# Kernel optimization log

Hardware: AMD Instinct MI355X
Metric: run time of the kernel (lower is better)

The kernel has to match this reference:

```python
import jax, jax.numpy as jnp
import numpy as np

VOCAB, DIM = 100000, 300
B, L = 4096, 200
HIDDEN, OUT = 1000, 3


def setup_inputs() -> dict:
    key = jax.random.key(0)
    k_emb, k_x, k_len, k_w1, k_b1, k_w2, k_b2 = jax.random.split(key, 7)
    emb_table = jax.random.normal(k_emb, (VOCAB, DIM), dtype=jnp.float32)
    x = jax.random.randint(k_x, (B, L), 0, VOCAB)
    lengths = jax.random.randint(k_len, (B,), 1, L + 1)  # >=1 to avoid div-by-zero
    W1 = jax.random.normal(k_w1, (2 * DIM, HIDDEN), dtype=jnp.float32) * 0.02
    b1 = jax.random.normal(k_b1, (HIDDEN,), dtype=jnp.float32) * 0.02
    W2 = jax.random.normal(k_w2, (HIDDEN, OUT), dtype=jnp.float32) * 0.02
    b2 = jax.random.normal(k_b2, (OUT,), dtype=jnp.float32) * 0.02
    return {"emb_table": emb_table, "W1": W1, "b1": b1, "W2": W2, "b2": b2,
            "x": x, "lengths": lengths}


def reference(emb_table, W1, b1, W2, b2, x, lengths):
    emb = emb_table[x]                                   # [B, L, D] gather
    # Faithful to original: mean uses sum over ALL positions (incl. padding)
    mean_pooled = jnp.sum(emb, axis=1) / lengths[:, None].astype(emb.dtype)  # [B, D]
    # Max only over the first `length` real tokens
    mask = jnp.arange(L)[None, :] < lengths[:, None]     # [B, L]
    neg_inf = jnp.array(-jnp.inf, dtype=emb.dtype)
    max_pooled = jnp.max(jnp.where(mask[:, :, None], emb, neg_inf), axis=1)  # [B, D]
    rep = jnp.concatenate([mean_pooled, max_pooled], axis=1)  # [B, 2D]
    h = jax.nn.relu(rep @ W1 + b1)                       # [B, 1000]
    return h @ W2 + b2                                   # [B, OUT]
```

## Files before the change

kernel.cpp:

```cpp
#include <hip/hip_runtime.h>
#include <math.h>

#define VOCAB  100000
#define DIM    300
#define IDIM   320
#define BB     4096
#define LL     200
#define HIDDEN 1000
#define OUTC   3
#define KT     19
#define NT     64
#define MTILES (BB / 16)

#define QSCALE (6.0f / 127.0f)
#define QINV   (127.0f / 6.0f)

#define W1_BLKS   ((KT * NT * 64 + 255) / 256)
#define INIT_BLKS ((BB * OUTC + 255) / 256)
#define CONV_BLKS ((VOCAB * 20 + 255) / 256)

typedef __attribute__((ext_vector_type(8))) short  short8;
typedef __attribute__((ext_vector_type(4))) float  floatx4;
typedef __attribute__((ext_vector_type(2))) unsigned short ushort2v;

__device__ inline ushort f2bf(float f) {
    union { float f; unsigned u; } v; v.f = f;
    unsigned u = v.u;
    u += 0x7fffu + ((u >> 16) & 1u);
    return (ushort)(u >> 16);
}
__device__ inline float4 f4max(float4 a, float4 b) {
    return make_float4(fmaxf(a.x, b.x), fmaxf(a.y, b.y), fmaxf(a.z, b.z), fmaxf(a.w, b.w));
}
__device__ inline float4 f4add(float4 a, float4 b) {
    return make_float4(a.x + b.x, a.y + b.y, a.z + b.z, a.w + b.w);
}
__device__ inline unsigned pkmax16(unsigned a, unsigned b) {
    union { unsigned u; ushort2v v; } x, y, r;
    x.u = a; y.u = b;
    r.v = __builtin_elementwise_max(x.v, y.v);
    return r.u;
}

__device__ inline int a_slot(int k, int ml) {
    const int kt = k >> 5, kk = k & 31;
    return ((kt << 6) + ml + ((kk >> 3) << 4)) * 8 + (kk & 7);
}

__device__ inline unsigned q4(float a, float b, float c, float d) {
    int q0 = min(max(__float2int_rn(a * QINV) + 128, 0), 255);
    int q1 = min(max(__float2int_rn(b * QINV) + 128, 0), 255);
    int q2 = min(max(__float2int_rn(c * QINV) + 128, 0), 255);
    int q3 = min(max(__float2int_rn(d * QINV) + 128, 0), 255);
    return (unsigned)q0 | ((unsigned)q1 << 8) | ((unsigned)q2 << 16) | ((unsigned)q3 << 24);
}

__global__ __launch_bounds__(256) void prep_all(
    const float* __restrict__ emb, unsigned char* __restrict__ embQ,
    const float* __restrict__ W1,  ushort* __restrict__ w1p,
    const float* __restrict__ b2,  float* __restrict__ out)
{
    const int bid = blockIdx.x;
    const int tid = threadIdx.x;
    if (bid < W1_BLKS) {
        const int g = bid * 256 + tid;
        if (g >= KT * NT * 64) return;
        const int lane = g & 63;
        const int nt   = (g >> 6) & (NT - 1);
        const int kt   = g >> 12;
        const int n    = nt * 16 + (lane & 15);
        const int kb   = kt * 32 + ((lane >> 4) << 3);
        short8 v;
        #pragma unroll
        for (int j = 0; j < 8; ++j) {
            const int k = kb + j;
            const float f = (k < 600 && n < HIDDEN) ? W1[k * HIDDEN + n] : 0.f;
            v[j] = (short)f2bf(f);
        }
        ((short8*)w1p)[g] = v;
    } else if (bid < W1_BLKS + INIT_BLKS) {
        const int g = (bid - W1_BLKS) * 256 + tid;
        if (g < BB * OUTC) out[g] = b2[g % OUTC];
    } else {
        const int g = (bid - W1_BLKS - INIT_BLKS) * 256 + tid;
        if (g >= VOCAB * 20) return;
        const int row = g / 20;
        const int c   = g - row * 20;
        const float4* rp = (const float4*)(emb + (size_t)row * DIM);
        uint4 o;
        unsigned* ow = (unsigned*)&o;
        #pragma unroll
        for (int v = 0; v < 4; ++v) {
            const int fi = 4 * c + v;
            float4 f = (fi < 75) ? rp[fi] : make_float4(0.f, 0.f, 0.f, 0.f);
            ow[v] = q4(f.x, f.y, f.z, f.w);
        }
        *(uint4*)(embQ + (size_t)g * 16) = o;
    }
}

__global__ __launch_bounds__(256, 8) void gather_pool_i8(
    const unsigned char* __restrict__ embQ,
    const int*           __restrict__ x,
    const int*           __restrict__ lengths,
    ushort*              __restrict__ repA)
{
    __shared__ int      xS[LL];
    __shared__ unsigned pS[3][20][8];
    __shared__ unsigned pM[3][20][8];

    const int tid  = threadIdx.x;
    const int lane = tid & 63;
    const int wave = tid >> 6;
    const int row  = blockIdx.x;

    for (int i = tid; i < LL; i += 256) xS[i] = x[row * LL + i];
    const int len = lengths[row];
    __syncthreads();

    const int  t0   = wave * 50;
    const int  vmax = min(max(len - t0, 0), 50);
    const bool ga   = (lane < 20);
    const bool ld   = (lane < 40);
    const int  lg   = ga ? lane : (lane - 20);

    unsigned sLo[4], sHi[4], mLo[4], mHi[4];
    #pragma unroll
    for (int w = 0; w < 4; ++w) { sLo[w] = sHi[w] = 0u; mLo[w] = mHi[w] = 0u; }

    uint4 raw = make_uint4(0, 0, 0, 0);
    const int full = vmax >> 1;
    int p = 0;
    for (; p < full; ++p) {
        const int tA  = t0 + 2 * p;
        const int idx = ga ? xS[tA] : xS[tA + 1];
        if (ld) raw = *(const uint4*)(embQ + (size_t)idx * IDIM + 16 * lg);
        const unsigned* ww = (const unsigned*)&raw;
        #pragma unroll
        for (int w = 0; w < 4; ++w) {
            const unsigned u  = ww[w];
            const unsigned lo = u & 0x00FF00FFu;
            const unsigned hi = (u >> 8) & 0x00FF00FFu;
            sLo[w] += lo;  sHi[w] += hi;
            mLo[w] = pkmax16(mLo[w], lo);
            mHi[w] = pkmax16(mHi[w], hi);
        }
    }
    if (vmax & 1) {
        const int tA  = t0 + 2 * p;
        const int idx = ga ? xS[tA] : xS[tA + 1];
        if (ld) raw = *(const uint4*)(embQ + (size_t)idx * IDIM + 16 * lg);
        const unsigned* ww = (const unsigned*)&raw;
        #pragma unroll
        for (int w = 0; w < 4; ++w) {
            const unsigned u  = ww[w];
            const unsigned lo = u & 0x00FF00FFu;
            const unsigned hi = (u >> 8) & 0x00FF00FFu;
            sLo[w] += lo;  sHi[w] += hi;
            if (ga) {
                mLo[w] = pkmax16(mLo[w], lo);
                mHi[w] = pkmax16(mHi[w], hi);
            }
        }
        ++p;
    }
    for (; p < 25; ++p) {
        const int tA  = t0 + 2 * p;
        const int idx = ga ? xS[tA] : xS[tA + 1];
        if (ld) raw = *(const uint4*)(embQ + (size_t)idx * IDIM + 16 * lg);
        const unsigned* ww = (const unsigned*)&raw;
        #pragma unroll
        for (int w = 0; w < 4; ++w) {
            const unsigned u = ww[w];
            sLo[w] += u & 0x00FF00FFu;
            sHi[w] += (u >> 8) & 0x00FF00FFu;
        }
    }

    {
        const int src = ga ? (lane + 20) : lane;
        #pragma unroll
        for (int w = 0; w < 4; ++w) {
            sLo[w] += (unsigned)__shfl((int)sLo[w], src);
            sHi[w] += (unsigned)__shfl((int)sHi[w], src);
            mLo[w] = pkmax16(mLo[w], (unsigned)__shfl((int)mLo[w], src));
            mHi[w] = pkmax16(mHi[w], (unsigned)__shfl((int)mHi[w], src));
        }
    }

    if (wave != 0 && ga) {
        #pragma unroll
        for (int w = 0; w < 4; ++w) {
            pS[wave - 1][lane][w]     = sLo[w];
            pS[wave - 1][lane][4 + w] = sHi[w];
            pM[wave - 1][lane][w]     = mLo[w];
            pM[wave - 1][lane][4 + w] = mHi[w];
        }
    }
    __syncthreads();
    if (wave == 0 && ga) {
        #pragma unroll
        for (int wv = 0; wv < 3; ++wv)
            #pragma unroll
            for (int w = 0; w < 4; ++w) {
                sLo[w] += pS[wv][lane][w];
                sHi[w] += pS[wv][lane][4 + w];
                mLo[w] = pkmax16(mLo[w], pM[wv][lane][w]);
                mHi[w] = pkmax16(mHi[w], pM[wv][lane][4 + w]);
            }

        float s[16], m[16];
        #pragma unroll
        for (int w = 0; w < 4; ++w) {
            s[4*w+0] = (float)(sLo[w] & 0xFFFFu);
            s[4*w+2] = (float)(sLo[w] >> 16);
            s[4*w+1] = (float)(sHi[w] & 0xFFFFu);
            s[4*w+3] = (float)(sHi[w] >> 16);
            m[4*w+0] = (float)(mLo[w] & 0xFFFFu);
            m[4*w+2] = (float)(mLo[w] >> 16);
            m[4*w+1] = (float)(mHi[w] & 0xFFFFu);
            m[4*w+3] = (float)(mHi[w] >> 16);
        }

        const float c1 = QSCALE / (float)len;
        const int mt = row >> 4;
        const int ml = row & 15;
        ushort* rb = repA + (size_t)mt * (KT * 512);

        ushort mv[16];
        #pragma unroll
        for (int j = 0; j < 16; ++j) mv[j] = f2bf((m[j] - 128.f) * QSCALE);

        if (lane < 18) {
            #pragma unroll
            for (int h = 0; h < 2; ++h) {
                short8 q;
                #pragma unroll
                for (int j = 0; j < 8; ++j)
                    q[j] = (short)f2bf((s[8*h + j] - 25600.f) * c1);
                *(short8*)(rb + a_slot(16 * lane + 8 * h, ml)) = q;
            }
            #pragma unroll
            for (int h = 0; h < 2; ++h) {
                const int k0 = 300 + 16 * lane + 8 * h;
                *(ushort4*)(rb + a_slot(k0, ml)) =
                    make_ushort4(mv[8*h+0], mv[8*h+1], mv[8*h+2], mv[8*h+3]);
                *(ushort4*)(rb + a_slot(k0 + 4, ml)) =
                    make_ushort4(mv[8*h+4], mv[8*h+5], mv[8*h+6], mv[8*h+7]);
            }
        } else if (lane == 18) {
            short8 q;
            #pragma unroll
            for (int j = 0; j < 8; ++j) q[j] = (short)f2bf((s[j] - 25600.f) * c1);
            *(short8*)(rb + a_slot(288, ml)) = q;
            *(ushort4*)(rb + a_slot(296, ml)) =
                make_ushort4(f2bf((s[8] - 25600.f) * c1), f2bf((s[9] - 25600.f) * c1),
                             f2bf((s[10] - 25600.f) * c1), f2bf((s[11] - 25600.f) * c1));
            *(ushort4*)(rb + a_slot(588, ml)) = make_ushort4(mv[0], mv[1], mv[2], mv[3]);
            *(ushort4*)(rb + a_slot(592, ml)) = make_ushort4(mv[4], mv[5], mv[6], mv[7]);
            *(ushort4*)(rb + a_slot(596, ml)) = make_ushort4(mv[8], mv[9], mv[10], mv[11]);
            *(ushort4*)(rb + a_slot(600, ml)) = make_ushort4(0, 0, 0, 0);
        } else {
            *(ushort4*)(rb + a_slot(604, ml)) = make_ushort4(0, 0, 0, 0);
        }
    }
}

__global__ __launch_bounds__(256, 8) void gather_pool_f32(
    const float* __restrict__ emb,
    const int*   __restrict__ x,
    const int*   __restrict__ lengths,
    ushort*      __restrict__ repA)
{
    __shared__ int    xS[LL];
    __shared__ float4 pS[3][75];
    __shared__ float4 pM[3][75];

    const int tid  = threadIdx.x;
    const int lane = tid & 63;
    const int wave = tid >> 6;
    const int row  = blockIdx.x;

    for (int i = tid; i < LL; i += 256) xS[i] = x[row * LL + i];
    const int len = lengths[row];
    __syncthreads();

    const int  t0   = wave * (LL / 4);
    const int  vmax = min(max(len - t0, 0), LL / 4);
    const bool tl   = (lane < 11);
    const float4 z4 = make_float4(0.f, 0.f, 0.f, 0.f);

    float4 s4 = z4, st = z4;
    float4 m4 = make_float4(-INFINITY, -INFINITY, -INFINITY, -INFINITY);
    float4 mt = m4;

    int t = 0;
    #pragma unroll 4
    for (; t < vmax; ++t) {
        const int idx = xS[t0 + t];
        const float4* rp = (const float4*)(emb + (size_t)idx * DIM);
        float4 a = rp[lane];
        float4 b = tl ? rp[64 + lane] : z4;
        s4 = f4add(s4, a); st = f4add(st, b);
        m4 = f4max(m4, a); mt = f4max(mt, b);
    }
    #pragma unroll 4
    for (; t < LL / 4; ++t) {
        const int idx = xS[t0 + t];
        const float4* rp = (const float4*)(emb + (size_t)idx * DIM);
        float4 a = rp[lane];
        float4 b = tl ? rp[64 + lane] : z4;
        s4 = f4add(s4, a); st = f4add(st, b);
    }

    if (wave != 0) {
        pS[wave - 1][lane] = s4; pM[wave - 1][lane] = m4;
        if (tl) { pS[wave - 1][64 + lane] = st; pM[wave - 1][64 + lane] = mt; }
    }
    __syncthreads();
    if (wave == 0) {
        #pragma unroll
        for (int w = 0; w < 3; ++w) {
            s4 = f4add(s4, pS[w][lane]); m4 = f4max(m4, pM[w][lane]);
            if (tl) { st = f4add(st, pS[w][64 + lane]); mt = f4max(mt, pM[w][64 + lane]); }
        }
        const float inv = 1.0f / (float)len;
        const int mtile = row >> 4;
        const int ml    = row & 15;
        ushort* rb = repA + (size_t)mtile * (KT * 512);
        {
            ushort4 q = make_ushort4(f2bf(s4.x*inv), f2bf(s4.y*inv), f2bf(s4.z*inv), f2bf(s4.w*inv));
            *(ushort4*)(rb + a_slot(4 * lane, ml)) = q;
        }
        {
            ushort4 q = make_ushort4(f2bf(m4.x), f2bf(m4.y), f2bf(m4.z), f2bf(m4.w));
            *(ushort4*)(rb + a_slot(300 + 4 * lane, ml)) = q;
        }
        if (tl) {
            ushort4 q1 = make_ushort4(f2bf(st.x*inv), f2bf(st.y*inv), f2bf(st.z*inv), f2bf(st.w*inv));
            *(ushort4*)(rb + a_slot(256 + 4 * lane, ml)) = q1;
            ushort4 q2 = make_ushort4(f2bf(mt.x), f2bf(mt.y), f2bf(mt.z), f2bf(mt.w));
            *(ushort4*)(rb + a_slot(556 + 4 * lane, ml)) = q2;
        }
        if (lane >= 56) rb[a_slot(600 + (lane - 56), ml)] = 0;
    }
}

__global__ __launch_bounds__(256, 4) void mlp_mfma(
    const ushort* __restrict__ w1p,
    const ushort* __restrict__ repA,
    const float*  __restrict__ b1,
    const float*  __restrict__ W2,
    float*        __restrict__ out)
{
    __shared__ short8 aS[KT * 64];
    __shared__ float  red[4][16][3];

    const int tid  = threadIdx.x;
    const int lane = tid & 63;
    const int wave = tid >> 6;
    const int mt   = blockIdx.x >> 2;
    const int q    = blockIdx.x & 3;

    {
        const short8* ap = (const short8*)(repA + (size_t)mt * (KT * 512));
        for (int i = tid; i < KT * 64; i += 256) aS[i] = ap[i];
    }
    __syncthreads();

    const int nt0 = q * 16 + wave * 4;
    const short8* bp = (const short8*)w1p;

    floatx4 acc[4];
    #pragma unroll
    for (int s = 0; s < 4; ++s) acc[s] = (floatx4){0.f, 0.f, 0.f, 0.f};

    #pragma unroll
    for (int kt = 0; kt < KT; ++kt) {
        const short8 av = aS[kt * 64 + lane];
        const short8 b0 = bp[(kt * NT + nt0 + 0) * 64 + lane];
        const short8 b1v = bp[(kt * NT + nt0 + 1) * 64 + lane];
        const short8 b2v = bp[(kt * NT + nt0 + 2) * 64 + lane];
        const short8 b3 = bp[(kt * NT + nt0 + 3) * 64 + lane];
        acc[0] = __builtin_amdgcn_mfma_f32_16x16x32_bf16(av, b0,  acc[0], 0, 0, 0);
        acc[1] = __builtin_amdgcn_mfma_f32_16x16x32_bf16(av, b1v, acc[1], 0, 0, 0);
        acc[2] = __builtin_amdgcn_mfma_f32_16x16x32_bf16(av, b2v, acc[2], 0, 0, 0);
        acc[3] = __builtin_amdgcn_mfma_f32_16x16x32_bf16(av, b3,  acc[3], 0, 0, 0);
    }

    float po[4][3];
    #pragma unroll
    for (int rg = 0; rg < 4; ++rg)
        #pragma unroll
        for (int j = 0; j < OUTC; ++j) po[rg][j] = 0.f;

    #pragma unroll
    for (int s = 0; s < 4; ++s) {
        const int n = (nt0 + s) * 16 + (lane & 15);
        const bool valid = (n < HIDDEN);
        const float bb  = b1[valid ? n : 0];
        const float w20 = valid ? W2[n * 3 + 0] : 0.f;
        const float w21 = valid ? W2[n * 3 + 1] : 0.f;
        const float w22 = valid ? W2[n * 3 + 2] : 0.f;
        #pragma unroll
        for (int rg = 0; rg < 4; ++rg) {
            const float h = fmaxf(acc[s][rg] + bb, 0.f);
            po[rg][0] = fmaf(h, w20, po[rg][0]);
            po[rg][1] = fmaf(h, w21, po[rg][1]);
            po[rg][2] = fmaf(h, w22, po[rg][2]);
        }
    }

    #pragma unroll
    for (int rg = 0; rg < 4; ++rg) {
        #pragma unroll
        for (int j = 0; j < OUTC; ++j) {
            float v = po[rg][j];
            v += __shfl_xor(v, 1);
            v += __shfl_xor(v, 2);
            v += __shfl_xor(v, 4);
            v += __shfl_xor(v, 8);
            if ((lane & 15) == 0) red[wave][(lane >> 4) * 4 + rg][j] = v;
        }
    }
    __syncthreads();

    if (tid < 16 * OUTC) {
        const int m = tid / OUTC, j = tid % OUTC;
        const float s = red[0][m][j] + red[1][m][j] + red[2][m][j] + red[3][m][j];
        atomicAdd(&out[(size_t)(mt * 16 + m) * OUTC + j], s);
    }
}

extern "C" void kernel_launch(void* const* d_in, const int* in_sizes, int n_in,
                              void* d_out, int out_size, void* d_ws, size_t ws_size,
                              hipStream_t stream) {
    const float* emb = (const float*)d_in[0];
    const float* W1  = (const float*)d_in[1];
    const float* b1  = (const float*)d_in[2];
    const float* W2  = (const float*)d_in[3];
    const float* b2  = (const float*)d_in[4];
    const int*   x   = (const int*)d_in[5];
    const int*   len = (const int*)d_in[6];
    float* out = (float*)d_out;

    const size_t W1P_ELTS  = (size_t)KT * NT * 64 * 8;
    const size_t REPA_ELTS = (size_t)MTILES * KT * 512;
    ushort* w1p  = (ushort*)d_ws;
    ushort* repA = w1p + W1P_ELTS;
    unsigned char* embQ = (unsigned char*)(repA + REPA_ELTS);
    const size_t need = (W1P_ELTS + REPA_ELTS) * 2 + (size_t)VOCAB * IDIM;
    const bool doConv = (ws_size >= need);

    const int prepGrid = W1_BLKS + INIT_BLKS + (doConv ? CONV_BLKS : 0);
    hipLaunchKernelGGL(prep_all, dim3(prepGrid), dim3(256), 0, stream,
                       emb, embQ, W1, w1p, b2, out);
    if (doConv) {
        hipLaunchKernelGGL(gather_pool_i8, dim3(BB), dim3(256), 0, stream,
                           embQ, x, len, repA);
    } else {
        hipLaunchKernelGGL(gather_pool_f32, dim3(BB), dim3(256), 0, stream,
                           emb, x, len, repA);
    }
    hipLaunchKernelGGL(mlp_mfma, dim3(MTILES * 4), dim3(256), 0, stream,
                       w1p, repA, b1, W2, out);
}
```

Before: 256.0 us.

## Gather three tokens per wave with register double-buffered loads and masked max

```diff
diff --git a/kernel.cpp b/kernel.cpp
--- a/kernel.cpp
+++ b/kernel.cpp
@@ -86,13 +86,14 @@
         if (g >= VOCAB * 20) return;
         const int row = g / 20;
         const int c   = g - row * 20;
-        const float4* rp = (const float4*)(emb + (size_t)row * DIM);
+        const floatx4* rp = (const floatx4*)(emb + (size_t)row * DIM);
         uint4 o;
         unsigned* ow = (unsigned*)&o;
         #pragma unroll
         for (int v = 0; v < 4; ++v) {
             const int fi = 4 * c + v;
-            float4 f = (fi < 75) ? rp[fi] : make_float4(0.f, 0.f, 0.f, 0.f);
+            floatx4 f = (fi < 75) ? __builtin_nontemporal_load(rp + fi)
+                                  : (floatx4){0.f, 0.f, 0.f, 0.f};
             ow[v] = q4(f.x, f.y, f.z, f.w);
         }
         *(uint4*)(embQ + (size_t)g * 16) = o;
@@ -120,22 +121,23 @@
 
     const int  t0   = wave * 50;
     const int  vmax = min(max(len - t0, 0), 50);
+    const int  tok  = (lane >= 20) + (lane >= 40);
+    const int  lg   = lane - 20 * tok;
     const bool ga   = (lane < 20);
-    const bool ld   = (lane < 40);
-    const int  lg   = ga ? lane : (lane - 20);
+    const bool ld3  = (lane < 60);
+    const bool ld2  = (lane < 40);
+
+    const int pm_all = vmax / 3;
+    const int pm_any = (vmax + 2) / 3;
 
     unsigned sLo[4], sHi[4], mLo[4], mHi[4];
     #pragma unroll
     for (int w = 0; w < 4; ++w) { sLo[w] = sHi[w] = 0u; mLo[w] = mHi[w] = 0u; }
 
-    uint4 raw = make_uint4(0, 0, 0, 0);
-    const int full = vmax >> 1;
-    int p = 0;
-    for (; p < full; ++p) {
-        const int tA  = t0 + 2 * p;
-        const int idx = ga ? xS[tA] : xS[tA + 1];
-        if (ld) raw = *(const uint4*)(embQ + (size_t)idx * IDIM + 16 * lg);
-        const unsigned* ww = (const unsigned*)&raw;
+    const unsigned char* colp = embQ + 16 * lg;
+
+    auto sumMax = [&](const uint4& v) {
+        const unsigned* ww = (const unsigned*)&v;
         #pragma unroll
         for (int w = 0; w < 4; ++w) {
             const unsigned u  = ww[w];
@@ -145,46 +147,80 @@
             mLo[w] = pkmax16(mLo[w], lo);
             mHi[w] = pkmax16(mHi[w], hi);
         }
-    }
-    if (vmax & 1) {
-        const int tA  = t0 + 2 * p;
-        const int idx = ga ? xS[tA] : xS[tA + 1];
-        if (ld) raw = *(const uint4*)(embQ + (size_t)idx * IDIM + 16 * lg);
-        const unsigned* ww = (const unsigned*)&raw;
+    };
+    auto sumMask = [&](const uint4& v, unsigned mk) {
+        const unsigned* ww = (const unsigned*)&v;
         #pragma unroll
         for (int w = 0; w < 4; ++w) {
             const unsigned u  = ww[w];
             const unsigned lo = u & 0x00FF00FFu;
             const unsigned hi = (u >> 8) & 0x00FF00FFu;
             sLo[w] += lo;  sHi[w] += hi;
-            if (ga) {
-                mLo[w] = pkmax16(mLo[w], lo);
-                mHi[w] = pkmax16(mHi[w], hi);
-            }
-        }
-        ++p;
-    }
-    for (; p < 25; ++p) {
-        const int tA  = t0 + 2 * p;
-        const int idx = ga ? xS[tA] : xS[tA + 1];
-        if (ld) raw = *(const uint4*)(embQ + (size_t)idx * IDIM + 16 * lg);
-        const unsigned* ww = (const unsigned*)&raw;
+            mLo[w] = pkmax16(mLo[w], lo & mk);
+            mHi[w] = pkmax16(mHi[w], hi & mk);
+        }
+    };
+    auto sumOnly = [&](const uint4& v) {
+        const unsigned* ww = (const unsigned*)&v;
         #pragma unroll
         for (int w = 0; w < 4; ++w) {
             const unsigned u = ww[w];
             sLo[w] += u & 0x00FF00FFu;
             sHi[w] += (u >> 8) & 0x00FF00FFu;
         }
-    }
-
+    };
+
+    uint4 cur = make_uint4(0, 0, 0, 0);
+    uint4 nxt = make_uint4(0, 0, 0, 0);
+    if (ld3) {
+        const int idx = xS[t0 + tok];
+        cur = *(const uint4*)(colp + (size_t)idx * IDIM);
+    }
+
+    #pragma unroll 2
+    for (int p = 0; p < 16; ++p) {
+        if (p < 15) {
+            if (ld3) {
+                const int idx = xS[t0 + 3 * (p + 1) + tok];
+                nxt = *(const uint4*)(colp + (size_t)idx * IDIM);
+            }
+        } else {
+            nxt = make_uint4(0, 0, 0, 0);
+            if (ld2) {
+                const int idx = xS[t0 + 48 + tok];
+                nxt = *(const uint4*)(colp + (size_t)idx * IDIM);
+            }
+        }
+        if (p < pm_all) {
+            sumMax(cur);
+        } else if (p < pm_any) {
+            const unsigned mk = (3 * p + tok < vmax) ? 0xFFFFFFFFu : 0u;
+            sumMask(cur, mk);
+        } else {
+            sumOnly(cur);
+        }
+        cur = nxt;
+    }
     {
-        const int src = ga ? (lane + 20) : lane;
+        const unsigned mk = (48 + tok < vmax) ? 0xFFFFFFFFu : 0u;
+        sumMask(cur, mk);
+    }
+
+    {
         #pragma unroll
         for (int w = 0; w < 4; ++w) {
-            sLo[w] += (unsigned)__shfl((int)sLo[w], src);
-            sHi[w] += (unsigned)__shfl((int)sHi[w], src);
-            mLo[w] = pkmax16(mLo[w], (unsigned)__shfl((int)mLo[w], src));
-            mHi[w] = pkmax16(mHi[w], (unsigned)__shfl((int)mHi[w], src));
+            const unsigned sa = (unsigned)__shfl((int)sLo[w], lg + 20);
+            const unsigned sb = (unsigned)__shfl((int)sLo[w], lg + 40);
+            const unsigned ha = (unsigned)__shfl((int)sHi[w], lg + 20);
+            const unsigned hb = (unsigned)__shfl((int)sHi[w], lg + 40);
+            sLo[w] += sa + sb;
+            sHi[w] += ha + hb;
+            const unsigned ma = (unsigned)__shfl((int)mLo[w], lg + 20);
+            const unsigned mb = (unsigned)__shfl((int)mLo[w], lg + 40);
+            const unsigned xa = (unsigned)__shfl((int)mHi[w], lg + 20);
+            const unsigned xb = (unsigned)__shfl((int)mHi[w], lg + 40);
+            mLo[w] = pkmax16(mLo[w], pkmax16(ma, mb));
+            mHi[w] = pkmax16(mHi[w], pkmax16(xa, xb));
         }
     }
 
```

New measurement: 264.7 us. 1.03x slower.

## Split int8 embedding table into column slabs and gather per-slab blocks

Applied to the files above, without the earlier changes.

```diff
diff --git a/kernel.cpp b/kernel.cpp
--- a/kernel.cpp
+++ b/kernel.cpp
@@ -3,7 +3,6 @@
 
 #define VOCAB  100000
 #define DIM    300
-#define IDIM   320
 #define BB     4096
 #define LL     200
 #define HIDDEN 1000
@@ -19,6 +18,8 @@
 #define INIT_BLKS ((BB * OUTC + 255) / 256)
 #define CONV_BLKS ((VOCAB * 20 + 255) / 256)
 
+#define SLABDW (VOCAB * 10)
+
 typedef __attribute__((ext_vector_type(8))) short  short8;
 typedef __attribute__((ext_vector_type(4))) float  floatx4;
 typedef __attribute__((ext_vector_type(2))) unsigned short ushort2v;
@@ -56,7 +57,7 @@
 }
 
 __global__ __launch_bounds__(256) void prep_all(
-    const float* __restrict__ emb, unsigned char* __restrict__ embQ,
+    const float* __restrict__ emb, unsigned* __restrict__ embQ,
     const float* __restrict__ W1,  ushort* __restrict__ w1p,
     const float* __restrict__ b2,  float* __restrict__ out)
 {
@@ -87,139 +88,158 @@
         const int row = g / 20;
         const int c   = g - row * 20;
         const float4* rp = (const float4*)(emb + (size_t)row * DIM);
-        uint4 o;
-        unsigned* ow = (unsigned*)&o;
         #pragma unroll
         for (int v = 0; v < 4; ++v) {
             const int fi = 4 * c + v;
             float4 f = (fi < 75) ? rp[fi] : make_float4(0.f, 0.f, 0.f, 0.f);
-            ow[v] = q4(f.x, f.y, f.z, f.w);
-        }
-        *(uint4*)(embQ + (size_t)g * 16) = o;
-    }
-}
-
-__global__ __launch_bounds__(256, 8) void gather_pool_i8(
-    const unsigned char* __restrict__ embQ,
-    const int*           __restrict__ x,
-    const int*           __restrict__ lengths,
-    ushort*              __restrict__ repA)
+            const unsigned o  = q4(f.x, f.y, f.z, f.w);
+            const int      sl = fi / 10;
+            const int      dw = fi - sl * 10;
+            embQ[(size_t)sl * SLABDW + row * 10 + dw] = o;
+        }
+    }
+}
+
+__global__ __launch_bounds__(128, 8) void gather_pool_i8(
+    const unsigned* __restrict__ embQ,
+    const int*      __restrict__ x,
+    const int*      __restrict__ lengths,
+    ushort*         __restrict__ repA)
 {
     __shared__ int      xS[LL];
-    __shared__ unsigned pS[3][20][8];
-    __shared__ unsigned pM[3][20][8];
+    __shared__ unsigned pX[5][8];
 
     const int tid  = threadIdx.x;
     const int lane = tid & 63;
     const int wave = tid >> 6;
-    const int row  = blockIdx.x;
-
-    for (int i = tid; i < LL; i += 256) xS[i] = x[row * LL + i];
+    const int row  = blockIdx.x >> 3;
+    const int s    = blockIdx.x & 7;
+
+    for (int i = tid; i < LL; i += 128) xS[i] = x[row * LL + i];
     const int len = lengths[row];
     __syncthreads();
 
-    const int  t0   = wave * 50;
-    const int  vmax = min(max(len - t0, 0), 50);
-    const bool ga   = (lane < 20);
-    const bool ld   = (lane < 40);
-    const int  lg   = ga ? lane : (lane - 20);
-
-    unsigned sLo[4], sHi[4], mLo[4], mHi[4];
-    #pragma unroll
-    for (int w = 0; w < 4; ++w) { sLo[w] = sHi[w] = 0u; mLo[w] = mHi[w] = 0u; }
-
-    uint4 raw = make_uint4(0, 0, 0, 0);
-    const int full = vmax >> 1;
+    const int  slot = lane % 5;
+    const int  tg   = lane / 5;
+    const bool act  = (lane < 60);
+
+    const int t0   = wave * 100;
+    const int vmax = min(max(len - t0, 0), 100);
+    const int pm_all = vmax / 12;
+    const int pm_any = (vmax + 11) / 12;
+
+    const unsigned* sb = embQ + (size_t)s * SLABDW + 2 * slot;
+
+    unsigned sL[2] = {0u, 0u}, sH[2] = {0u, 0u};
+    unsigned mL[2] = {0u, 0u}, mH[2] = {0u, 0u};
+
     int p = 0;
-    for (; p < full; ++p) {
-        const int tA  = t0 + 2 * p;
-        const int idx = ga ? xS[tA] : xS[tA + 1];
-        if (ld) raw = *(const uint4*)(embQ + (size_t)idx * IDIM + 16 * lg);
-        const unsigned* ww = (const unsigned*)&raw;
-        #pragma unroll
-        for (int w = 0; w < 4; ++w) {
+    for (; p < pm_all; ++p) {
+        const int t   = 12 * p + tg;
+        const int idx = xS[t0 + t];
+        uint2 v = make_uint2(0u, 0u);
+        if (act) v = *(const uint2*)(sb + (size_t)idx * 10);
+        const unsigned* ww = (const unsigned*)&v;
+        #pragma unroll
+        for (int w = 0; w < 2; ++w) {
             const unsigned u  = ww[w];
             const unsigned lo = u & 0x00FF00FFu;
             const unsigned hi = (u >> 8) & 0x00FF00FFu;
-            sLo[w] += lo;  sHi[w] += hi;
-            mLo[w] = pkmax16(mLo[w], lo);
-            mHi[w] = pkmax16(mHi[w], hi);
-        }
-    }
-    if (vmax & 1) {
-        const int tA  = t0 + 2 * p;
-        const int idx = ga ? xS[tA] : xS[tA + 1];
-        if (ld) raw = *(const uint4*)(embQ + (size_t)idx * IDIM + 16 * lg);
-        const unsigned* ww = (const unsigned*)&raw;
-        #pragma unroll
-        for (int w = 0; w < 4; ++w) {
+            sL[w] += lo;  sH[w] += hi;
+            mL[w] = pkmax16(mL[w], lo);
+            mH[w] = pkmax16(mH[w], hi);
+        }
+    }
+    for (; p < pm_any; ++p) {
+        const int  t  = 12 * p + tg;
+        const bool on = act && (t < 100);
+        const int idx = xS[t0 + (on ? t : 0)];
+        uint2 v = make_uint2(0u, 0u);
+        if (on) v = *(const uint2*)(sb + (size_t)idx * 10);
+        const unsigned mk = (t < vmax) ? 0xFFFFFFFFu : 0u;
+        const unsigned* ww = (const unsigned*)&v;
+        #pragma unroll
+        for (int w = 0; w < 2; ++w) {
             const unsigned u  = ww[w];
             const unsigned lo = u & 0x00FF00FFu;
             const unsigned hi = (u >> 8) & 0x00FF00FFu;
-            sLo[w] += lo;  sHi[w] += hi;
-            if (ga) {
-                mLo[w] = pkmax16(mLo[w], lo);
-                mHi[w] = pkmax16(mHi[w], hi);
-            }
-        }
-        ++p;
-    }
-    for (; p < 25; ++p) {
-        const int tA  = t0 + 2 * p;
-        const int idx = ga ? xS[tA] : xS[tA + 1];
-        if (ld) raw = *(const uint4*)(embQ + (size_t)idx * IDIM + 16 * lg);
-        const unsigned* ww = (const unsigned*)&raw;
-        #pragma unroll
-        for (int w = 0; w < 4; ++w) {
+            sL[w] += lo;  sH[w] += hi;
+            mL[w] = pkmax16(mL[w], lo & mk);
+            mH[w] = pkmax16(mH[w], hi & mk);
+        }
+    }
+    for (; p < 9; ++p) {
+        const int  t  = 12 * p + tg;
+        const bool on = act && (t < 100);
+        const int idx = xS[t0 + (on ? t : 0)];
+        uint2 v = make_uint2(0u, 0u);
+        if (on) v = *(const uint2*)(sb + (size_t)idx * 10);
+        const unsigned* ww = (const unsigned*)&v;
+        #pragma unroll
+        for (int w = 0; w < 2; ++w) {
             const unsigned u = ww[w];
-            sLo[w] += u & 0x00FF00FFu;
-            sHi[w] += (u >> 8) & 0x00FF00FFu;
+            sL[w] += u & 0x00FF00FFu;
+            sH[w] += (u >> 8) & 0x00FF00FFu;
         }
     }
 
     {
-        const int src = ga ? (lane + 20) : lane;
-        #pragma unroll
-        for (int w = 0; w < 4; ++w) {
-            sLo[w] += (unsigned)__shfl((int)sLo[w], src);
-            sHi[w] += (unsigned)__shfl((int)sHi[w], src);
-            mLo[w] = pkmax16(mLo[w], (unsigned)__shfl((int)mLo[w], src));
-            mHi[w] = pkmax16(mHi[w], (unsigned)__shfl((int)mHi[w], src));
-        }
-    }
-
-    if (wave != 0 && ga) {
-        #pragma unroll
-        for (int w = 0; w < 4; ++w) {
-            pS[wave - 1][lane][w]     = sLo[w];
-            pS[wave - 1][lane][4 + w] = sHi[w];
-            pM[wave - 1][lane][w]     = mLo[w];
-            pM[wave - 1][lane][4 + w] = mHi[w];
-        }
-    }
-    __syncthreads();
-    if (wave == 0 && ga) {
-        #pragma unroll
-        for (int wv = 0; wv < 3; ++wv)
-            #pragma unroll
-            for (int w = 0; w < 4; ++w) {
-                sLo[w] += pS[wv][lane][w];
-                sHi[w] += pS[wv][lane][4 + w];
-                mLo[w] = pkmax16(mLo[w], pM[wv][lane][w]);
-                mHi[w] = pkmax16(mHi[w], pM[wv][lane][4 + w]);
-            }
-
-        float s[16], m[16];
-        #pragma unroll
-        for (int w = 0; w < 4; ++w) {
-            s[4*w+0] = (float)(sLo[w] & 0xFFFFu);
-            s[4*w+2] = (float)(sLo[w] >> 16);
-            s[4*w+1] = (float)(sHi[w] & 0xFFFFu);
-            s[4*w+3] = (float)(sHi[w] >> 16);
-            m[4*w+0] = (float)(mLo[w] & 0xFFFFu);
-            m[4*w+2] = (float)(mLo[w] >> 16);
-            m[4*w+1] = (float)(mHi[w] & 0xFFFFu);
-            m[4*w+3] = (float)(mHi[w] >> 16);
+        const int s1 = slot + 5 * min(tg + 4, 11);
+        const int s2 = slot + 5 * min(tg + 8, 11);
+        #pragma unroll
+        for (int w = 0; w < 2; ++w) {
+            const unsigned a1 = (unsigned)__shfl((int)sL[w], s1);
+            const unsigned a2 = (unsigned)__shfl((int)sL[w], s2);
+            const unsigned b1 = (unsigned)__shfl((int)sH[w], s1);
+            const unsigned b2 = (unsigned)__shfl((int)sH[w], s2);
+            const unsigned c1v = (unsigned)__shfl((int)mL[w], s1);
+            const unsigned c2v = (unsigned)__shfl((int)mL[w], s2);
+            const unsigned d1 = (unsigned)__shfl((int)mH[w], s1);
+            const unsigned d2 = (unsigned)__shfl((int)mH[w], s2);
+            sL[w] += a1 + a2;
+            sH[w] += b1 + b2;
+            mL[w] = pkmax16(mL[w], pkmax16(c1v, c2v));
+            mH[w] = pkmax16(mH[w], pkmax16(d1, d2));
+        }
+    }
+    {
+        const int sc = slot + 5 * min(tg + 2, 11);
+        #pragma unroll
+        for (int w = 0; w < 2; ++w) {
+            sL[w] += (unsigned)__shfl((int)sL[w], sc);
+            sH[w] += (unsigned)__shfl((int)sH[w], sc);
+            mL[w] = pkmax16(mL[w], (unsigned)__shfl((int)mL[w], sc));
+            mH[w] = pkmax16(mH[w], (unsigned)__shfl((int)mH[w], sc));
+        }
+    }
+    {
+        const int sc = slot + 5 * min(tg + 1, 11);
+        #pragma unroll
+        for (int w = 0; w < 2; ++w) {
+            sL[w] += (unsigned)__shfl((int)sL[w], sc);
+            sH[w] += (unsigned)__shfl((int)sH[w], sc);
+            mL[w] = pkmax16(mL[w], (unsigned)__shfl((int)mL[w], sc));
+            mH[w] = pkmax16(mH[w], (unsigned)__shfl((int)mH[w], sc));
+        }
+    }
+
+    if (wave == 1 && lane < 5) {
+        #pragma unroll
+        for (int w = 0; w < 2; ++w) {
+            pX[lane][w]     = sL[w];
+            pX[lane][2 + w] = sH[w];
+            pX[lane][4 + w] = mL[w];
+            pX[lane][6 + w] = mH[w];
+        }
+    }
+    __syncthreads();
+    if (wave == 0 && lane < 5) {
+        #pragma unroll
+        for (int w = 0; w < 2; ++w) {
+            sL[w] += pX[lane][w];
+            sH[w] += pX[lane][2 + w];
+            mL[w] = pkmax16(mL[w], pX[lane][4 + w]);
+            mH[w] = pkmax16(mH[w], pX[lane][6 + w]);
         }
 
         const float c1 = QSCALE / (float)len;
@@ -227,41 +247,28 @@
         const int ml = row & 15;
         ushort* rb = repA + (size_t)mt * (KT * 512);
 
-        ushort mv[16];
-        #pragma unroll
-        for (int j = 0; j < 16; ++j) mv[j] = f2bf((m[j] - 128.f) * QSCALE);
-
-        if (lane < 18) {
-            #pragma unroll
-            for (int h = 0; h < 2; ++h) {
-                short8 q;
-                #pragma unroll
-                for (int j = 0; j < 8; ++j)
-                    q[j] = (short)f2bf((s[8*h + j] - 25600.f) * c1);
-                *(short8*)(rb + a_slot(16 * lane + 8 * h, ml)) = q;
+        #pragma unroll
+        for (int w = 0; w < 2; ++w) {
+            const int k0 = 40 * s + 8 * slot + 4 * w;
+            float S[4], M[4];
+            S[0] = (float)(sL[w] & 0xFFFFu);  S[2] = (float)(sL[w] >> 16);
+            S[1] = (float)(sH[w] & 0xFFFFu);  S[3] = (float)(sH[w] >> 16);
+            M[0] = (float)(mL[w] & 0xFFFFu);  M[2] = (float)(mL[w] >> 16);
+            M[1] = (float)(mH[w] & 0xFFFFu);  M[3] = (float)(mH[w] >> 16);
+            if (k0 < 300) {
+                ushort4 qm = make_ushort4(
+                    f2bf((S[0] - 25600.f) * c1), f2bf((S[1] - 25600.f) * c1),
+                    f2bf((S[2] - 25600.f) * c1), f2bf((S[3] - 25600.f) * c1));
+                *(ushort4*)(rb + a_slot(k0, ml)) = qm;
+                ushort4 qx = make_ushort4(
+                    f2bf((M[0] - 128.f) * QSCALE), f2bf((M[1] - 128.f) * QSCALE),
+                    f2bf((M[2] - 128.f) * QSCALE), f2bf((M[3] - 128.f) * QSCALE));
+                *(ushort4*)(rb + a_slot(300 + k0, ml)) = qx;
+            } else if (s == 7 && slot == 2 && w == 1) {
+                *(ushort4*)(rb + a_slot(600, ml)) = make_ushort4(0, 0, 0, 0);
+            } else if (s == 7 && slot == 3 && w == 0) {
+                *(ushort4*)(rb + a_slot(604, ml)) = make_ushort4(0, 0, 0, 0);
             }
-            #pragma unroll
-            for (int h = 0; h < 2; ++h) {
-                const int k0 = 300 + 16 * lane + 8 * h;
-                *(ushort4*)(rb + a_slot(k0, ml)) =
-                    make_ushort4(mv[8*h+0], mv[8*h+1], mv[8*h+2], mv[8*h+3]);
-                *(ushort4*)(rb + a_slot(k0 + 4, ml)) =
-                    make_ushort4(mv[8*h+4], mv[8*h+5], mv[8*h+6], mv[8*h+7]);
-            }
-        } else if (lane == 18) {
-            short8 q;
-            #pragma unroll
-            for (int j = 0; j < 8; ++j) q[j] = (short)f2bf((s[j] - 25600.f) * c1);
-            *(short8*)(rb + a_slot(288, ml)) = q;
-            *(ushort4*)(rb + a_slot(296, ml)) =
-                make_ushort4(f2bf((s[8] - 25600.f) * c1), f2bf((s[9] - 25600.f) * c1),
-                             f2bf((s[10] - 25600.f) * c1), f2bf((s[11] - 25600.f) * c1));
-            *(ushort4*)(rb + a_slot(588, ml)) = make_ushort4(mv[0], mv[1], mv[2], mv[3]);
-            *(ushort4*)(rb + a_slot(592, ml)) = make_ushort4(mv[4], mv[5], mv[6], mv[7]);
-            *(ushort4*)(rb + a_slot(596, ml)) = make_ushort4(mv[8], mv[9], mv[10], mv[11]);
-            *(ushort4*)(rb + a_slot(600, ml)) = make_ushort4(0, 0, 0, 0);
-        } else {
-            *(ushort4*)(rb + a_slot(604, ml)) = make_ushort4(0, 0, 0, 0);
         }
     }
 }
@@ -448,15 +455,15 @@
     const size_t REPA_ELTS = (size_t)MTILES * KT * 512;
     ushort* w1p  = (ushort*)d_ws;
     ushort* repA = w1p + W1P_ELTS;
-    unsigned char* embQ = (unsigned char*)(repA + REPA_ELTS);
-    const size_t need = (W1P_ELTS + REPA_ELTS) * 2 + (size_t)VOCAB * IDIM;
+    unsigned* embQ = (unsigned*)(repA + REPA_ELTS);
+    const size_t need = (W1P_ELTS + REPA_ELTS) * 2 + (size_t)8 * SLABDW * 4;
     const bool doConv = (ws_size >= need);
 
     const int prepGrid = W1_BLKS + INIT_BLKS + (doConv ? CONV_BLKS : 0);
     hipLaunchKernelGGL(prep_all, dim3(prepGrid), dim3(256), 0, stream,
                        emb, embQ, W1, w1p, b2, out);
     if (doConv) {
-        hipLaunchKernelGGL(gather_pool_i8, dim3(BB), dim3(256), 0, stream,
+        hipLaunchKernelGGL(gather_pool_i8, dim3(BB * 8), dim3(128), 0, stream,
                            embQ, x, len, repA);
     } else {
         hipLaunchKernelGGL(gather_pool_f32, dim3(BB), dim3(256), 0, stream,
```

Result: slower. 285.2 us (+11.4%).
